# Performance work log

Measured on AMD Instinct MI355X. Metric: run time of the kernel, lower is better.

Reference implementation:

```python
import jax, jax.numpy as jnp
import numpy as np

L_K = 6  # number of nearest neighbors (matches module-level L_K)
N_POINTS = 4096


def setup_inputs() -> dict:
    key = jax.random.key(0)
    k1, k2, k3, k4 = jax.random.split(key, 4)
    input_t = jax.random.normal(k1, (1, 3, N_POINTS), dtype=jnp.float32)
    sf_t = jax.random.normal(k2, (1, 3, N_POINTS), dtype=jnp.float32) * 0.1
    y1 = jax.random.normal(k3, (1, 3, N_POINTS), dtype=jnp.float32)
    pred = jax.random.normal(k4, (1, 3, N_POINTS), dtype=jnp.float32)
    return {"input_t": input_t, "sf_t": sf_t, "y1": y1, "pred": pred}


def _kabsch(pc, recon):
    # Standard Kabsch rigid-transform estimation (pc, recon: [N,3]).
    cp = pc.mean(axis=0)
    cr = recon.mean(axis=0)
    H = (pc - cp).T @ (recon - cr)  # [3,3] cross-covariance
    U, S, Vt = jnp.linalg.svd(H)
    d = jnp.sign(jnp.linalg.det(Vt.T @ U.T))
    # R = V diag(1,1,d) U^T  (reflection fix)
    R = Vt.T @ (jnp.stack([jnp.float32(1.0), jnp.float32(1.0), d])[:, None] * U.T)
    t = cr - R @ cp
    return R, t


def _knn_laplace(centers, ref, k):
    # centers: [N,3] query points (x1); ref: [M,3] cloud to gather neighbors from.
    # Matches: squared_dist over all pairs, topk smallest along ref dim,
    # grouping gather, then Laplacian differencing normalized by (k-1).
    d2 = jnp.sum((centers[:, None, :] - ref[None, :, :]) ** 2, axis=-1)  # [N,M]
    _, idx = jax.lax.top_k(-d2, k)  # k smallest distances -> neighbor indices [N,k]
    grouped = ref[idx]  # [N,k,3] gather
    return jnp.sum(grouped - centers[:, None, :], axis=1) / float(k - 1)  # [N,3]


def reference(input_t, sf_t, y1, pred):
    # Rigid reconstruction: we use a single cluster covering all points
    # (deterministic stand-in for the CPU-side DBSCAN clustering), so the
    # whole cloud is rigidly reconstructed via Kabsch, then detached
    # (original code calls .detach() on the Kabsch reconstruction).
    pc = input_t[0].T        # [N,3]
    recon = pc + sf_t[0].T   # [N,3]
    R, t = _kabsch(pc, recon)
    rigid_recon = jax.lax.stop_gradient(pc @ R.T + t)  # [N,3]

    yT = y1[0].T  # [N,3]
    laplace_y = _knn_laplace(rigid_recon, yT, L_K)          # cross-cloud kNN Laplacian
    laplace_x = _knn_laplace(rigid_recon, rigid_recon, L_K)  # self kNN Laplacian
    laplace_reduced = laplace_x - laplace_y  # [N,3]

    # Single cluster = all points: subtract mean Laplacian difference.
    rigid_refine = rigid_recon - jnp.mean(laplace_reduced, axis=0)  # [N,3]

    # L1 loss (mean reduction) vs student prediction.
    return jnp.mean(jnp.abs(rigid_refine - pred[0].T))
```

## Files before the change

### kernel.cpp

```cpp
#include <hip/hip_runtime.h>
#include <math.h>

#define NP 4096
#define KNN 6
#define NCHUNK 16
#define CHUNK 256

typedef unsigned int u32;
typedef unsigned long long u64;

__device__ inline double wave_reduce(double v) {
#pragma unroll
  for (int o = 32; o > 0; o >>= 1) v += __shfl_down(v, o);
  return v;
}

__device__ inline float det3f(const float M[3][3]) {
  return M[0][0]*(M[1][1]*M[2][2]-M[1][2]*M[2][1])
       - M[0][1]*(M[1][0]*M[2][2]-M[1][2]*M[2][0])
       + M[0][2]*(M[1][0]*M[2][1]-M[1][1]*M[2][0]);
}

#define TOP6_INSERT_ILP(key)                                          \
  { u32 m0 = max(b0, key), m1 = max(b1, key), m2 = max(b2, key),      \
        m3 = max(b3, key), m4 = max(b4, key);                         \
    b0 = min(b0, key); b1 = min(b1, m0); b2 = min(b2, m1);            \
    b3 = min(b3, m2); b4 = min(b4, m3); b5 = min(b5, m4); }

__global__ __launch_bounds__(256) void k1_kabsch(const float* __restrict__ in,
                                                 const float* __restrict__ sf,
                                                 float* __restrict__ Rt,
                                                 u32* __restrict__ counter) {
  const int tid = threadIdx.x;
  const int lane = tid & 63, wv = tid >> 6;
  double acc[15];
#pragma unroll
  for (int q = 0; q < 15; ++q) acc[q] = 0.0;
  for (int i = tid; i < NP; i += 256) {
    double px = in[i], py = in[NP + i], pz = in[2*NP + i];
    double qx = px + (double)sf[i];
    double qy = py + (double)sf[NP + i];
    double qz = pz + (double)sf[2*NP + i];
    acc[0] += px; acc[1] += py; acc[2] += pz;
    acc[3] += qx; acc[4] += qy; acc[5] += qz;
    acc[6] += px*qx; acc[7]  += px*qy; acc[8]  += px*qz;
    acc[9] += py*qx; acc[10] += py*qy; acc[11] += py*qz;
    acc[12]+= pz*qx; acc[13] += pz*qy; acc[14] += pz*qz;
  }
  __shared__ double wred[4][15];
#pragma unroll
  for (int q = 0; q < 15; ++q) {
    double v = wave_reduce(acc[q]);
    if (lane == 0) wred[wv][q] = v;
  }
  __syncthreads();
  if (tid == 0) {
    double tot[15];
    for (int q = 0; q < 15; ++q)
      tot[q] = wred[0][q] + wred[1][q] + wred[2][q] + wred[3][q];
    const double invN = 1.0 / (double)NP;
    double cp[3] = { tot[0]*invN, tot[1]*invN, tot[2]*invN };
    double cr[3] = { tot[3]*invN, tot[4]*invN, tot[5]*invN };
    float H[3][3];
    for (int a = 0; a < 3; ++a)
      for (int b = 0; b < 3; ++b)
        H[a][b] = (float)(tot[6 + a*3 + b] - (double)NP * cp[a] * cr[b]);
    float A[3][3];
    for (int a = 0; a < 3; ++a)
      for (int b = 0; b < 3; ++b)
        A[a][b] = H[0][a]*H[0][b] + H[1][a]*H[1][b] + H[2][a]*H[2][b];
    float V[3][3] = {{1,0,0},{0,1,0},{0,0,1}};
    const int PQ[3][2] = {{0,1},{0,2},{1,2}};
    for (int sweep = 0; sweep < 8; ++sweep) {
      for (int r = 0; r < 3; ++r) {
        const int p = PQ[r][0], q = PQ[r][1];
        float apq = A[p][q];
        if (fabsf(apq) > 1e-30f) {
          float theta = (A[q][q] - A[p][p]) / (2.0f * apq);
          float tt = copysignf(1.0f, theta) / (fabsf(theta) + sqrtf(theta*theta + 1.0f));
          float c = 1.0f / sqrtf(tt*tt + 1.0f);
          float s = tt * c;
          for (int k = 0; k < 3; ++k) { float akp=A[k][p], akq=A[k][q]; A[k][p]=c*akp - s*akq; A[k][q]=s*akp + c*akq; }
          for (int k = 0; k < 3; ++k) { float apk=A[p][k], aqk=A[q][k]; A[p][k]=c*apk - s*aqk; A[q][k]=s*apk + c*aqk; }
          for (int k = 0; k < 3; ++k) { float vkp=V[k][p], vkq=V[k][q]; V[k][p]=c*vkp - s*vkq; V[k][q]=s*vkp + c*vkq; }
        }
      }
    }
    int ord[3] = {0,1,2};
    for (int a = 0; a < 2; ++a)
      for (int b = a + 1; b < 3; ++b)
        if (A[ord[b]][ord[b]] > A[ord[a]][ord[a]]) { int t2 = ord[a]; ord[a] = ord[b]; ord[b] = t2; }
    float Vc[3][3], Uc[3][3];
    for (int j = 0; j < 3; ++j) {
      const int e = ord[j];
      float lam = A[e][e] > 0.0f ? A[e][e] : 0.0f;
      float sv = sqrtf(lam);
      float isv = sv > 1e-20f ? 1.0f / sv : 0.0f;
      for (int a = 0; a < 3; ++a) Vc[a][j] = V[a][e];
      for (int a = 0; a < 3; ++a)
        Uc[a][j] = (H[a][0]*Vc[0][j] + H[a][1]*Vc[1][j] + H[a][2]*Vc[2][j]) * isv;
    }
    float dd = (det3f(Uc) * det3f(Vc)) >= 0.0f ? 1.0f : -1.0f;
    float R[3][3];
    for (int a = 0; a < 3; ++a)
      for (int b = 0; b < 3; ++b)
        R[a][b] = Vc[a][0]*Uc[b][0] + Vc[a][1]*Uc[b][1] + dd * Vc[a][2]*Uc[b][2];
    for (int a = 0; a < 3; ++a) {
      Rt[a*3+0] = R[a][0]; Rt[a*3+1] = R[a][1]; Rt[a*3+2] = R[a][2];
      Rt[9+a] = (float)(cr[a] - ((double)R[a][0]*cp[0] + (double)R[a][1]*cp[1]
                                 + (double)R[a][2]*cp[2]));
    }
    *counter = 0u;
  }
}

__global__ __launch_bounds__(256) void k2_scan(const float* __restrict__ in,
                                               const float* __restrict__ ycloud,
                                               const float* __restrict__ Rt,
                                               u32* __restrict__ part,
                                               float* __restrict__ rx,
                                               float* __restrict__ ry,
                                               float* __restrict__ rz) {
  __shared__ float4 sc[CHUNK];
  __shared__ float Rts[12];
  const int tid = threadIdx.x;
  const int chunk = blockIdx.x, cblk = blockIdx.y, cloud = blockIdx.z;
  if (tid < 12) Rts[tid] = Rt[tid];
  __syncthreads();
  const float r0=Rts[0], r1=Rts[1], r2=Rts[2];
  const float r3=Rts[3], r4=Rts[4], r5=Rts[5];
  const float r6=Rts[6], r7=Rts[7], r8=Rts[8];
  const float t0=Rts[9], t1=Rts[10], t2=Rts[11];
  const int j0 = chunk * CHUNK;
  {
    const int jj = j0 + tid;
    float a, b, c;
    if (cloud == 0) {
      float px = in[jj], py = in[NP + jj], pz = in[2*NP + jj];
      a = fmaf(r0, px, fmaf(r1, py, fmaf(r2, pz, t0)));
      b = fmaf(r3, px, fmaf(r4, py, fmaf(r5, pz, t1)));
      c = fmaf(r6, px, fmaf(r7, py, fmaf(r8, pz, t2)));
      if (chunk == cblk) { rx[jj] = a; ry[jj] = b; rz[jj] = c; }
    } else {
      a = ycloud[jj]; b = ycloud[NP + jj]; c = ycloud[2*NP + jj];
    }
    sc[tid] = make_float4(a, b, c, fmaf(a, a, fmaf(b, b, c * c)));
  }
  const int ci = cblk * CHUNK + tid;
  float cx, cy, cz;
  {
    float px = in[ci], py = in[NP + ci], pz = in[2*NP + ci];
    cx = fmaf(r0, px, fmaf(r1, py, fmaf(r2, pz, t0)));
    cy = fmaf(r3, px, fmaf(r4, py, fmaf(r5, pz, t1)));
    cz = fmaf(r6, px, fmaf(r7, py, fmaf(r8, pz, t2)));
  }
  const float ax = -2.f*cx, ay = -2.f*cy, az = -2.f*cz;
  __syncthreads();
  u32 b0=~0u, b1=~0u, b2=~0u, b3=~0u, b4=~0u, b5=~0u;
#pragma unroll 8
  for (int j = 0; j < CHUNK; ++j) {
    float4 c = sc[j];
    float s = fmaf(c.x, ax, fmaf(c.y, ay, fmaf(c.z, az, c.w)));
    u32 bits = __float_as_uint(s);
    u32 u = bits ^ ((u32)((int)bits >> 31) | 0x80000000u);
    u32 key = (u & 0xFFFFF000u) | (u32)(j0 + j);
    TOP6_INSERT_ILP(key);
  }
  u32* o = part + (size_t)(cloud * NCHUNK + chunk) * KNN * NP + ci;
  o[0*NP] = b0; o[1*NP] = b1; o[2*NP] = b2;
  o[3*NP] = b3; o[4*NP] = b4; o[5*NP] = b5;
}

__global__ __launch_bounds__(256) void k3_merge_final(const u32* __restrict__ part,
                                                      const float* __restrict__ rx,
                                                      const float* __restrict__ ry,
                                                      const float* __restrict__ rz,
                                                      const float* __restrict__ ycloud,
                                                      const float* __restrict__ pred,
                                                      double* __restrict__ blockpart,
                                                      u32* __restrict__ counter,
                                                      float* __restrict__ out) {
  const int tid = threadIdx.x;
  const int lane = tid & 63, wv = tid >> 6;
  const int cloud = blockIdx.x >> 4, cblk = blockIdx.x & 15;
  const int ci = cblk * 256 + tid;
  u32 b0=~0u, b1=~0u, b2=~0u, b3=~0u, b4=~0u, b5=~0u;
  for (int c = 0; c < NCHUNK; ++c) {
    const u32* p = part + (size_t)(cloud * NCHUNK + c) * KNN * NP + ci;
#pragma unroll
    for (int e = 0; e < KNN; ++e) {
      u32 key = p[(size_t)e * NP];
      TOP6_INSERT_ILP(key);
    }
  }
  u32 bk[KNN] = { b0, b1, b2, b3, b4, b5 };
  float s0 = 0.f, s1 = 0.f, s2 = 0.f;
  if (cloud == 0) {
#pragma unroll
    for (int k = 0; k < KNN; ++k) {
      int idx = (int)(bk[k] & 0xFFFu);
      s0 += rx[idx]; s1 += ry[idx]; s2 += rz[idx];
    }
  } else {
#pragma unroll
    for (int k = 0; k < KNN; ++k) {
      int idx = (int)(bk[k] & 0xFFFu);
      s0 += ycloud[idx]; s1 += ycloud[NP + idx]; s2 += ycloud[2*NP + idx];
    }
  }
  const double sgn = cloud ? -1.0 : 1.0;
  double v0 = wave_reduce(sgn * (double)s0);
  double v1 = wave_reduce(sgn * (double)s1);
  double v2 = wave_reduce(sgn * (double)s2);
  __shared__ double wred[4][3];
  __shared__ int lastFlag;
  if (lane == 0) { wred[wv][0] = v0; wred[wv][1] = v1; wred[wv][2] = v2; }
  __syncthreads();
  if (tid == 0) {
    for (int q = 0; q < 3; ++q) {
      double B = wred[0][q] + wred[1][q] + wred[2][q] + wred[3][q];
      atomicExch((u64*)&blockpart[blockIdx.x * 3 + q], (u64)__double_as_longlong(B));
    }
    __threadfence();
    u32 t = atomicAdd(counter, 1u);
    lastFlag = (t == 31u);
  }
  __syncthreads();
  if (!lastFlag) return;

  __shared__ double bp[96];
  __threadfence();
  if (tid < 96)
    bp[tid] = __longlong_as_double((long long)atomicAdd((u64*)&blockpart[tid], 0ULL));
  __syncthreads();
  __shared__ float m[3];
  if (tid == 0) {
    double a0 = 0.0, a1 = 0.0, a2 = 0.0;
    for (int b = 0; b < 32; ++b) {
      a0 += bp[b*3 + 0]; a1 += bp[b*3 + 1]; a2 += bp[b*3 + 2];
    }
    const double sc = 0.2 / (double)NP;
    m[0] = (float)(a0 * sc); m[1] = (float)(a1 * sc); m[2] = (float)(a2 * sc);
  }
  __syncthreads();
  const float m0 = m[0], m1 = m[1], m2 = m[2];
  double s = 0.0;
  for (int i = tid; i < NP; i += 256) {
    s += (double)fabsf(rx[i] - m0 - pred[i]);
    s += (double)fabsf(ry[i] - m1 - pred[NP + i]);
    s += (double)fabsf(rz[i] - m2 - pred[2*NP + i]);
  }
  double v = wave_reduce(s);
  __shared__ double fred[4];
  if (lane == 0) fred[wv] = v;
  __syncthreads();
  if (tid == 0)
    out[0] = (float)((fred[0] + fred[1] + fred[2] + fred[3]) / (3.0 * (double)NP));
}

extern "C" void kernel_launch(void* const* d_in, const int* in_sizes, int n_in,
                              void* d_out, int out_size, void* d_ws, size_t ws_size,
                              hipStream_t stream) {
  const float* in   = (const float*)d_in[0];
  const float* sf   = (const float*)d_in[1];
  const float* y1   = (const float*)d_in[2];
  const float* pred = (const float*)d_in[3];

  u32* part = (u32*)d_ws;
  double* blockpart = (double*)(part + (size_t)2*NCHUNK*KNN*NP);
  u32* counter = (u32*)(blockpart + 96);
  float* Rt = (float*)(counter + 4);
  float* rx = Rt + 12;
  float* ry = rx + NP;
  float* rz = ry + NP;

  k1_kabsch<<<1, 256, 0, stream>>>(in, sf, Rt, counter);
  k2_scan<<<dim3(NCHUNK, 16, 2), 256, 0, stream>>>(in, y1, Rt, part, rx, ry, rz);
  k3_merge_final<<<32, 256, 0, stream>>>(part, rx, ry, rz, y1, pred,
                                         blockpart, counter, (float*)d_out);
}
```

Measured before the change: 56.06 us.

## Pack transformed and y clouds as float4 in Kabsch kernel, drop LDS staging in scan

The single-block Kabsch kernel now applies the rigid transform itself and writes both candidate clouds as packed float4 (x,y,z,|p|^2) to workspace. The scan kernel no longer recomputes transforms or stages candidates in LDS. It reads uniform float4 candidates straight from global memory, which the compiler can turn into scalar loads. The merge kernel gathers neighbors with a single float4 load. The cost is that the serial one-block kernel does more work, and the inner scan loop now depends on global or cache latency instead of LDS.

```diff
diff --git a/kernel.cpp b/kernel.cpp
--- a/kernel.cpp
+++ b/kernel.cpp
@@ -27,10 +27,12 @@
     b0 = min(b0, key); b1 = min(b1, m0); b2 = min(b2, m1);            \
     b3 = min(b3, m2); b4 = min(b4, m3); b5 = min(b5, m4); }
 
-__global__ __launch_bounds__(256) void k1_kabsch(const float* __restrict__ in,
-                                                 const float* __restrict__ sf,
-                                                 float* __restrict__ Rt,
-                                                 u32* __restrict__ counter) {
+__global__ __launch_bounds__(256) void k1_kabsch_pack(const float* __restrict__ in,
+                                                      const float* __restrict__ sf,
+                                                      const float* __restrict__ ycloud,
+                                                      float4* __restrict__ cand0,
+                                                      float4* __restrict__ cand1,
+                                                      u32* __restrict__ counter) {
   const int tid = threadIdx.x;
   const int lane = tid & 63, wv = tid >> 6;
   double acc[15];
@@ -54,6 +56,7 @@
     if (lane == 0) wred[wv][q] = v;
   }
   __syncthreads();
+  __shared__ float Rts[12];
   if (tid == 0) {
     double tot[15];
     for (int q = 0; q < 15; ++q)
@@ -106,60 +109,42 @@
       for (int b = 0; b < 3; ++b)
         R[a][b] = Vc[a][0]*Uc[b][0] + Vc[a][1]*Uc[b][1] + dd * Vc[a][2]*Uc[b][2];
     for (int a = 0; a < 3; ++a) {
-      Rt[a*3+0] = R[a][0]; Rt[a*3+1] = R[a][1]; Rt[a*3+2] = R[a][2];
-      Rt[9+a] = (float)(cr[a] - ((double)R[a][0]*cp[0] + (double)R[a][1]*cp[1]
-                                 + (double)R[a][2]*cp[2]));
+      Rts[a*3+0] = R[a][0]; Rts[a*3+1] = R[a][1]; Rts[a*3+2] = R[a][2];
+      Rts[9+a] = (float)(cr[a] - ((double)R[a][0]*cp[0] + (double)R[a][1]*cp[1]
+                                  + (double)R[a][2]*cp[2]));
     }
     *counter = 0u;
   }
-}
-
-__global__ __launch_bounds__(256) void k2_scan(const float* __restrict__ in,
-                                               const float* __restrict__ ycloud,
-                                               const float* __restrict__ Rt,
-                                               u32* __restrict__ part,
-                                               float* __restrict__ rx,
-                                               float* __restrict__ ry,
-                                               float* __restrict__ rz) {
-  __shared__ float4 sc[CHUNK];
-  __shared__ float Rts[12];
-  const int tid = threadIdx.x;
-  const int chunk = blockIdx.x, cblk = blockIdx.y, cloud = blockIdx.z;
-  if (tid < 12) Rts[tid] = Rt[tid];
   __syncthreads();
   const float r0=Rts[0], r1=Rts[1], r2=Rts[2];
   const float r3=Rts[3], r4=Rts[4], r5=Rts[5];
   const float r6=Rts[6], r7=Rts[7], r8=Rts[8];
   const float t0=Rts[9], t1=Rts[10], t2=Rts[11];
+  for (int i = tid; i < NP; i += 256) {
+    float px = in[i], py = in[NP + i], pz = in[2*NP + i];
+    float a = fmaf(r0, px, fmaf(r1, py, fmaf(r2, pz, t0)));
+    float b = fmaf(r3, px, fmaf(r4, py, fmaf(r5, pz, t1)));
+    float c = fmaf(r6, px, fmaf(r7, py, fmaf(r8, pz, t2)));
+    cand0[i] = make_float4(a, b, c, fmaf(a, a, fmaf(b, b, c * c)));
+    float yx = ycloud[i], yy = ycloud[NP + i], yz = ycloud[2*NP + i];
+    cand1[i] = make_float4(yx, yy, yz, fmaf(yx, yx, fmaf(yy, yy, yz * yz)));
+  }
+}
+
+__global__ __launch_bounds__(256) void k2_scan(const float4* __restrict__ cand0,
+                                               const float4* __restrict__ cand1,
+                                               u32* __restrict__ part) {
+  const int tid = threadIdx.x;
+  const int chunk = blockIdx.x, cblk = blockIdx.y, cloud = blockIdx.z;
   const int j0 = chunk * CHUNK;
-  {
-    const int jj = j0 + tid;
-    float a, b, c;
-    if (cloud == 0) {
-      float px = in[jj], py = in[NP + jj], pz = in[2*NP + jj];
-      a = fmaf(r0, px, fmaf(r1, py, fmaf(r2, pz, t0)));
-      b = fmaf(r3, px, fmaf(r4, py, fmaf(r5, pz, t1)));
-      c = fmaf(r6, px, fmaf(r7, py, fmaf(r8, pz, t2)));
-      if (chunk == cblk) { rx[jj] = a; ry[jj] = b; rz[jj] = c; }
-    } else {
-      a = ycloud[jj]; b = ycloud[NP + jj]; c = ycloud[2*NP + jj];
-    }
-    sc[tid] = make_float4(a, b, c, fmaf(a, a, fmaf(b, b, c * c)));
-  }
+  const float4* __restrict__ cand = cloud ? cand1 : cand0;
   const int ci = cblk * CHUNK + tid;
-  float cx, cy, cz;
-  {
-    float px = in[ci], py = in[NP + ci], pz = in[2*NP + ci];
-    cx = fmaf(r0, px, fmaf(r1, py, fmaf(r2, pz, t0)));
-    cy = fmaf(r3, px, fmaf(r4, py, fmaf(r5, pz, t1)));
-    cz = fmaf(r6, px, fmaf(r7, py, fmaf(r8, pz, t2)));
-  }
-  const float ax = -2.f*cx, ay = -2.f*cy, az = -2.f*cz;
-  __syncthreads();
+  const float4 ct = cand0[ci];
+  const float ax = -2.f*ct.x, ay = -2.f*ct.y, az = -2.f*ct.z;
   u32 b0=~0u, b1=~0u, b2=~0u, b3=~0u, b4=~0u, b5=~0u;
 #pragma unroll 8
   for (int j = 0; j < CHUNK; ++j) {
-    float4 c = sc[j];
+    float4 c = cand[j0 + j];
     float s = fmaf(c.x, ax, fmaf(c.y, ay, fmaf(c.z, az, c.w)));
     u32 bits = __float_as_uint(s);
     u32 u = bits ^ ((u32)((int)bits >> 31) | 0x80000000u);
@@ -172,10 +157,8 @@
 }
 
 __global__ __launch_bounds__(256) void k3_merge_final(const u32* __restrict__ part,
-                                                      const float* __restrict__ rx,
-                                                      const float* __restrict__ ry,
-                                                      const float* __restrict__ rz,
-                                                      const float* __restrict__ ycloud,
+                                                      const float4* __restrict__ cand0,
+                                                      const float4* __restrict__ cand1,
                                                       const float* __restrict__ pred,
                                                       double* __restrict__ blockpart,
                                                       u32* __restrict__ counter,
@@ -194,19 +177,12 @@
     }
   }
   u32 bk[KNN] = { b0, b1, b2, b3, b4, b5 };
+  const float4* __restrict__ g = cloud ? cand1 : cand0;
   float s0 = 0.f, s1 = 0.f, s2 = 0.f;
-  if (cloud == 0) {
-#pragma unroll
-    for (int k = 0; k < KNN; ++k) {
-      int idx = (int)(bk[k] & 0xFFFu);
-      s0 += rx[idx]; s1 += ry[idx]; s2 += rz[idx];
-    }
-  } else {
-#pragma unroll
-    for (int k = 0; k < KNN; ++k) {
-      int idx = (int)(bk[k] & 0xFFFu);
-      s0 += ycloud[idx]; s1 += ycloud[NP + idx]; s2 += ycloud[2*NP + idx];
-    }
+#pragma unroll
+  for (int k = 0; k < KNN; ++k) {
+    float4 nb = g[bk[k] & 0xFFFu];
+    s0 += nb.x; s1 += nb.y; s2 += nb.z;
   }
   const double sgn = cloud ? -1.0 : 1.0;
   double v0 = wave_reduce(sgn * (double)s0);
@@ -246,9 +222,10 @@
   const float m0 = m[0], m1 = m[1], m2 = m[2];
   double s = 0.0;
   for (int i = tid; i < NP; i += 256) {
-    s += (double)fabsf(rx[i] - m0 - pred[i]);
-    s += (double)fabsf(ry[i] - m1 - pred[NP + i]);
-    s += (double)fabsf(rz[i] - m2 - pred[2*NP + i]);
+    float4 rc = cand0[i];
+    s += (double)fabsf(rc.x - m0 - pred[i]);
+    s += (double)fabsf(rc.y - m1 - pred[NP + i]);
+    s += (double)fabsf(rc.z - m2 - pred[2*NP + i]);
   }
   double v = wave_reduce(s);
   __shared__ double fred[4];
@@ -269,13 +246,11 @@
   u32* part = (u32*)d_ws;
   double* blockpart = (double*)(part + (size_t)2*NCHUNK*KNN*NP);
   u32* counter = (u32*)(blockpart + 96);
-  float* Rt = (float*)(counter + 4);
-  float* rx = Rt + 12;
-  float* ry = rx + NP;
-  float* rz = ry + NP;
-
-  k1_kabsch<<<1, 256, 0, stream>>>(in, sf, Rt, counter);
-  k2_scan<<<dim3(NCHUNK, 16, 2), 256, 0, stream>>>(in, y1, Rt, part, rx, ry, rz);
-  k3_merge_final<<<32, 256, 0, stream>>>(part, rx, ry, rz, y1, pred,
+  float4* cand0 = (float4*)(counter + 4);
+  float4* cand1 = cand0 + NP;
+
+  k1_kabsch_pack<<<1, 256, 0, stream>>>(in, sf, y1, cand0, cand1, counter);
+  k2_scan<<<dim3(NCHUNK, 16, 2), 256, 0, stream>>>(cand0, cand1, part);
+  k3_merge_final<<<32, 256, 0, stream>>>(part, cand0, cand1, pred,
                                          blockpart, counter, (float*)d_out);
 }
```

New measurement: 64.28 us. 14.7% more time.
